# Optimization experiments

Hardware: AMD Instinct MI355X
Metric: run time of the kernel (lower is better)

Reference implementation:

```python
import jax, jax.numpy as jnp
import numpy as np

STRIDE = 1
PAD = 1
K = 3  # kernel size


def setup_inputs() -> dict:
    key = jax.random.key(0)
    k1, k2, k3, k4 = jax.random.split(key, 4)
    B, C, H, W, O = 4, 256, 64, 64, 256
    x = jax.random.normal(k1, (B, C, H, W), jnp.float32)
    offset = jax.random.normal(k2, (B, 2 * K * K, H, W), jnp.float32)
    mask = jax.random.uniform(k3, (B, K * K, H, W), jnp.float32)
    # kaiming-ish scale for the conv weight
    weight = jax.random.normal(k4, (O, C, K, K), jnp.float32) / np.float32(np.sqrt(C * K * K))
    return {"x": x, "offset": offset, "mask": mask, "weight": weight}


def _deform_conv2d(x, offset, mask, weight, stride=STRIDE, pad=PAD):
    """Modulated deformable conv v2 (torchvision deform_conv2d semantics)."""
    B, C, H, W = x.shape
    O, _, Kh, Kw = weight.shape
    KK = Kh * Kw
    Ho = (H + 2 * pad - Kh) // stride + 1
    Wo = (W + 2 * pad - Kw) // stride + 1

    # offset layout: [B, 2*KK, Ho, Wo], pairs are (dy, dx) per kernel tap
    off = offset.reshape(B, KK, 2, Ho, Wo)
    dy, dx = off[:, :, 0], off[:, :, 1]  # [B, KK, Ho, Wo]

    ki = (jnp.arange(KK) // Kw).astype(x.dtype)  # kernel row per tap
    kj = (jnp.arange(KK) % Kw).astype(x.dtype)   # kernel col per tap
    base_y = (jnp.arange(Ho) * stride - pad).astype(x.dtype)
    base_x = (jnp.arange(Wo) * stride - pad).astype(x.dtype)

    # sampling positions [B, KK, Ho, Wo]
    py = base_y[None, None, :, None] + ki[None, :, None, None] + dy
    px = base_x[None, None, None, :] + kj[None, :, None, None] + dx

    y0 = jnp.floor(py)
    x0 = jnp.floor(px)
    wy = py - y0  # fractional weights
    wx = px - x0
    y0i = y0.astype(jnp.int32)
    x0i = x0.astype(jnp.int32)

    x_bhwc = jnp.transpose(x, (0, 2, 3, 1))  # [B, H, W, C] for gathers
    b_idx = jnp.arange(B)[:, None, None, None]

    def gather(yi, xi):
        # zero outside the image (zero-padding bilinear sampling)
        valid = (yi >= 0) & (yi < H) & (xi >= 0) & (xi < W)
        v = x_bhwc[b_idx, jnp.clip(yi, 0, H - 1), jnp.clip(xi, 0, W - 1)]  # [B,KK,Ho,Wo,C]
        return v * valid[..., None].astype(x.dtype)

    one = jnp.asarray(1, x.dtype)
    sampled = (gather(y0i, x0i) * ((one - wy) * (one - wx))[..., None]
               + gather(y0i, x0i + 1) * ((one - wy) * wx)[..., None]
               + gather(y0i + 1, x0i) * (wy * (one - wx))[..., None]
               + gather(y0i + 1, x0i + 1) * (wy * wx)[..., None])

    sampled = sampled * mask.reshape(B, KK, Ho, Wo)[..., None]  # modulation

    # weighted accumulation == implicit GEMM over (c, kk)
    return jnp.einsum('bkhwc,ock->bohw', sampled, weight.reshape(O, C, KK))


def reference(x, offset, mask, weight):
    return _deform_conv2d(x, offset, mask, weight)
```

## Files before the change

### kernel.cpp

```cpp
#include <hip/hip_runtime.h>
#include <hip/hip_bf16.h>

#define CN 256
#define HN 64
#define WN 64
#define ON 256
#define KKN 9
#define HWN 4096
#define KDIM 2304
#define KC 288

using frag_ab = __attribute__((ext_vector_type(8))) short;
using frag_cd = __attribute__((ext_vector_type(4))) float;
using short4v = __attribute__((ext_vector_type(4))) short;
using int4v   = __attribute__((ext_vector_type(4))) int;
using float4v = __attribute__((ext_vector_type(4))) float;
using float2v = __attribute__((ext_vector_type(2))) float;
using uint2v  = __attribute__((ext_vector_type(2))) unsigned;

static __device__ inline short f2bf(float f) {
    union { float f; unsigned u; } v; v.f = f;
    unsigned r = v.u + 0x7fffu + ((v.u >> 16) & 1u);
    return (short)(r >> 16);
}

__global__ __launch_bounds__(256) void prep_kernel(const float* __restrict__ x,
                                                   const float* __restrict__ wsrc,
                                                   short* __restrict__ xb16,
                                                   short* __restrict__ wtb) {
    int bidx = blockIdx.x;
    int tid  = threadIdx.x;
    if (bidx < 1024) {
        __shared__ float tile[64][65];
        int b   = bidx >> 8;
        int rem = bidx & 255;
        int c0  = (rem >> 6) * 64;
        int p0  = (rem & 63) * 64;
        int tp = tid & 63, tc = tid >> 6;
        for (int i = 0; i < 16; ++i) {
            int c = tc + i * 4;
            tile[c][tp] = x[(b * CN + c0 + c) * HWN + p0 + tp];
        }
        __syncthreads();
        int tcc = tid & 63, tpp = tid >> 6;
        for (int i = 0; i < 16; ++i) {
            int p = tpp + i * 4;
            xb16[(b * HWN + p0 + p) * CN + c0 + tcc] = f2bf(tile[tcc][p]);
        }
    } else {
        int chunk = (bidx - 1024) * 256 + tid;
        int ob  = chunk / (KC * 64);
        int rem = chunk - ob * (KC * 64);
        int kc  = rem >> 6;
        int row = rem & 63;
        int o   = ob * 64 + row;
        int kk  = kc >> 5;
        int oct = kc & 31;
        frag_ab v;
        #pragma unroll
        for (int e = 0; e < 8; ++e)
            v[e] = f2bf(wsrc[(o * CN + oct * 8 + e) * 9 + kk]);
        *(frag_ab*)&wtb[(size_t)chunk * 8] = v;
    }
}

__global__ __launch_bounds__(512, 4) void fused_kernel(const short* __restrict__ xb16,
                                                       const short* __restrict__ wtb,
                                                       const float* __restrict__ offs,
                                                       const float* __restrict__ maskp,
                                                       float* __restrict__ out) {
    __shared__ struct {
        union {
            short Ab[2][8448];
            float outb[32 * 257];
        } mix;
        int desc[2304];
    } sm;
    int tid  = threadIdx.x;
    int m0   = blockIdx.x * 32;
    int b    = m0 >> 12;
    int h    = (m0 >> 6) & 63;
    int w0   = m0 & 63;
    int wv   = __builtin_amdgcn_readfirstlane(tid >> 6);
    int lane = tid & 63;
    int q    = lane >> 4, r = lane & 15;
    int wbase = 33 * (lane >> 1) * 8 + (lane & 1) * 4;
    int lane4 = lane * 4;
    int wv4   = wv * 4;

    if (tid < 288) {
        int kk = tid >> 5;
        int m  = tid & 31;
        int wc = w0 + m;
        int p  = h * 64 + wc;
        int ki = kk / 3, kj = kk - ki * 3;
        float dy = offs[(b * 18 + 2 * kk) * HWN + p];
        float dx = offs[(b * 18 + 2 * kk + 1) * HWN + p];
        float mv = maskp[(b * 9 + kk) * HWN + p];
        float py = (float)(h - 1 + ki) + dy;
        float px = (float)(wc - 1 + kj) + dx;
        float y0f = floorf(py), x0f = floorf(px);
        float wy = py - y0f, wx = px - x0f;
        int y0 = (int)y0f, x0 = (int)x0f;
        int4v cb; float4v cw;
        #pragma unroll
        for (int cy = 0; cy < 2; ++cy)
            #pragma unroll
            for (int cx = 0; cx < 2; ++cx) {
                int yy = y0 + cy, xx = x0 + cx;
                bool valid = (yy >= 0 && yy < HN && xx >= 0 && xx < WN);
                int yc = min(max(yy, 0), HN - 1);
                int xc = min(max(xx, 0), WN - 1);
                cb[cy * 2 + cx] = ((b * HN + yc) * WN + xc) * CN;
                float wgt = (cy ? wy : 1.f - wy) * (cx ? wx : 1.f - wx) * mv;
                cw[cy * 2 + cx] = valid ? wgt : 0.f;
            }
        int* dd = &sm.desc[tid * 8];
        *(int4v*)dd       = cb;
        *(float4v*)(dd + 4) = cw;
    }
    __syncthreads();

    frag_cd acc[2][2];
    #pragma unroll
    for (int i = 0; i < 2; ++i)
        #pragma unroll
        for (int j = 0; j < 2; ++j)
            acc[i][j] = (frag_cd){0.f, 0.f, 0.f, 0.f};

    short4v stg[4][4];
    float4v cwc[4];

    auto prefetch = [&](int kk1) {
        #pragma unroll
        for (int i = 0; i < 4; ++i) {
            int dbase = (kk1 * 32 + wv4 + i) * 8;
            int4v cb = *(const int4v*)&sm.desc[dbase];
            cwc[i]   = *(const float4v*)&sm.desc[dbase + 4];
            #pragma unroll
            for (int c = 0; c < 4; ++c)
                stg[i][c] = *(const short4v*)&xb16[cb[c] + lane4];
        }
    };

    prefetch(0);

    int jb = (wv & 1) * 2;
    int ob = wv >> 1;
    for (int kk = 0; kk < KKN; ++kk) {
        short* dst = sm.mix.Ab[kk & 1];
        #pragma unroll
        for (int i = 0; i < 4; ++i) {
            float4v cw = cwc[i];
            short4v res;
            #pragma unroll
            for (int g = 0; g < 2; ++g) {
                float2v a = (float2v){0.f, 0.f};
                #pragma unroll
                for (int c = 0; c < 4; ++c) {
                    uint2v uv = __builtin_bit_cast(uint2v, stg[i][c]);
                    unsigned uu = uv[g];
                    float2v f;
                    f.x = __builtin_bit_cast(float, uu << 16);
                    f.y = __builtin_bit_cast(float, uu & 0xffff0000u);
                    a += f * cw[c];
                }
                __hip_bfloat162 p2 = __float22bfloat162_rn(make_float2(a.x, a.y));
                res[2 * g]     = *(short*)&p2.x;
                res[2 * g + 1] = *(short*)&p2.y;
            }
            *(short4v*)&dst[wbase + (wv4 + i) * 8] = res;
        }
        if (kk < 8) prefetch(kk + 1);
        __syncthreads();
        #pragma unroll
        for (int ks = 0; ks < 8; ++ks) {
            frag_ab af[2], bf[2];
            #pragma unroll
            for (int i = 0; i < 2; ++i)
                af[i] = *(const frag_ab*)
                    &dst[(33 * (ks * 4 + q) + i * 16 + r) * 8];
            #pragma unroll
            for (int j = 0; j < 2; ++j)
                bf[j] = *(const frag_ab*)
                    &wtb[(((size_t)ob * KC + kk * 32 + ks * 4 + q) * 64
                          + (jb + j) * 16 + r) * 8];
            __builtin_amdgcn_s_setprio(1);
            #pragma unroll
            for (int i = 0; i < 2; ++i)
                #pragma unroll
                for (int j = 0; j < 2; ++j)
                    acc[i][j] = __builtin_amdgcn_mfma_f32_16x16x32_bf16(
                        af[i], bf[j], acc[i][j], 0, 0, 0);
            __builtin_amdgcn_s_setprio(0);
        }
    }
    __syncthreads();

    #pragma unroll
    for (int i = 0; i < 2; ++i)
        #pragma unroll
        for (int j = 0; j < 2; ++j) {
            int ml = i * 16 + q * 4;
            int ol = wv * 32 + j * 16 + r;
            sm.mix.outb[(ml + 0) * 257 + ol] = acc[i][j][0];
            sm.mix.outb[(ml + 1) * 257 + ol] = acc[i][j][1];
            sm.mix.outb[(ml + 2) * 257 + ol] = acc[i][j][2];
            sm.mix.outb[(ml + 3) * 257 + ol] = acc[i][j][3];
        }
    __syncthreads();
    {
        int ww = tid & 31;
        int og = tid >> 5;
        #pragma unroll
        for (int oo = 0; oo < 16; ++oo) {
            int o = oo * 16 + og;
            out[(((size_t)b * ON + o) * HN + h) * WN + w0 + ww] =
                sm.mix.outb[ww * 257 + o];
        }
    }
}

extern "C" void kernel_launch(void* const* d_in, const int* in_sizes, int n_in,
                              void* d_out, int out_size, void* d_ws, size_t ws_size,
                              hipStream_t stream) {
    const float* x      = (const float*)d_in[0];
    const float* offset = (const float*)d_in[1];
    const float* mask   = (const float*)d_in[2];
    const float* weight = (const float*)d_in[3];
    float* out = (float*)d_out;

    short* xb16 = (short*)d_ws;
    short* wtb  = (short*)((char*)d_ws + 8388608);

    hipLaunchKernelGGL(prep_kernel,  dim3(1312), dim3(256), 0, stream,
                       x, weight, xb16, wtb);
    hipLaunchKernelGGL(fused_kernel, dim3(512),  dim3(512), 0, stream,
                       xb16, wtb, offset, mask, out);
}
```

Before: 121.3 us.

## Enlarge fused block to a full 64-pixel row with 16 waves and register-prefetched weights

Each block of the fused kernel now covers a whole 64-pixel output row with 1024 threads (16 waves), and the grid drops from 512 to 256 blocks. Each wave now owns 16 output channels across all 64 pixels, so one weight fragment feeds four MFMAs instead of two. Weight fragments are double-buffered in registers, loaded two k-steps ahead, and the pre-MFMA __syncthreads becomes an LDS-only waitcnt plus a raw barrier. The cost is double the LDS per block, fewer blocks for the 256 CUs, and heavier register pressure under the 1024-thread launch bound.

```diff
diff --git a/kernel.cpp b/kernel.cpp
--- a/kernel.cpp
+++ b/kernel.cpp
@@ -64,41 +64,39 @@
     }
 }
 
-__global__ __launch_bounds__(512, 4) void fused_kernel(const short* __restrict__ xb16,
-                                                       const short* __restrict__ wtb,
-                                                       const float* __restrict__ offs,
-                                                       const float* __restrict__ maskp,
-                                                       float* __restrict__ out) {
+__global__ __launch_bounds__(1024, 4) void fused_kernel(const short* __restrict__ xb16,
+                                                        const short* __restrict__ wtb,
+                                                        const float* __restrict__ offs,
+                                                        const float* __restrict__ maskp,
+                                                        float* __restrict__ out) {
     __shared__ struct {
         union {
-            short Ab[2][8448];
-            float outb[32 * 257];
+            short Ab[2][16640];
+            float outb[64 * 257];
         } mix;
-        int desc[2304];
+        int desc[4608];
     } sm;
     int tid  = threadIdx.x;
-    int m0   = blockIdx.x * 32;
+    int m0   = blockIdx.x * 64;
     int b    = m0 >> 12;
     int h    = (m0 >> 6) & 63;
-    int w0   = m0 & 63;
     int wv   = __builtin_amdgcn_readfirstlane(tid >> 6);
     int lane = tid & 63;
     int q    = lane >> 4, r = lane & 15;
-    int wbase = 33 * (lane >> 1) * 8 + (lane & 1) * 4;
+    int wbase = 65 * (lane >> 1) * 8 + (lane & 1) * 4;
     int lane4 = lane * 4;
     int wv4   = wv * 4;
 
-    if (tid < 288) {
-        int kk = tid >> 5;
-        int m  = tid & 31;
-        int wc = w0 + m;
-        int p  = h * 64 + wc;
+    if (tid < 576) {
+        int kk = tid >> 6;
+        int m  = tid & 63;
+        int p  = h * 64 + m;
         int ki = kk / 3, kj = kk - ki * 3;
         float dy = offs[(b * 18 + 2 * kk) * HWN + p];
         float dx = offs[(b * 18 + 2 * kk + 1) * HWN + p];
         float mv = maskp[(b * 9 + kk) * HWN + p];
         float py = (float)(h - 1 + ki) + dy;
-        float px = (float)(wc - 1 + kj) + dx;
+        float px = (float)(m - 1 + kj) + dx;
         float y0f = floorf(py), x0f = floorf(px);
         float wy = py - y0f, wx = px - x0f;
         int y0 = (int)y0f, x0 = (int)x0f;
@@ -121,12 +119,10 @@
     }
     __syncthreads();
 
-    frag_cd acc[2][2];
+    frag_cd acc[4];
     #pragma unroll
-    for (int i = 0; i < 2; ++i)
-        #pragma unroll
-        for (int j = 0; j < 2; ++j)
-            acc[i][j] = (frag_cd){0.f, 0.f, 0.f, 0.f};
+    for (int i = 0; i < 4; ++i)
+        acc[i] = (frag_cd){0.f, 0.f, 0.f, 0.f};
 
     short4v stg[4][4];
     float4v cwc[4];
@@ -134,7 +130,7 @@
     auto prefetch = [&](int kk1) {
         #pragma unroll
         for (int i = 0; i < 4; ++i) {
-            int dbase = (kk1 * 32 + wv4 + i) * 8;
+            int dbase = (kk1 * 64 + wv4 + i) * 8;
             int4v cb = *(const int4v*)&sm.desc[dbase];
             cwc[i]   = *(const float4v*)&sm.desc[dbase + 4];
             #pragma unroll
@@ -143,12 +139,21 @@
         }
     };
 
+    int ob   = wv >> 2;
+    int orow = (wv & 3) * 16;
+    auto ld_bf = [&](int kk, int ks) {
+        return *(const frag_ab*)
+            &wtb[(((size_t)ob * KC + kk * 32 + ks * 4 + q) * 64
+                  + orow + r) * 8];
+    };
+
     prefetch(0);
 
-    int jb = (wv & 1) * 2;
-    int ob = wv >> 1;
     for (int kk = 0; kk < KKN; ++kk) {
         short* dst = sm.mix.Ab[kk & 1];
+        frag_ab bfx[2];
+        bfx[0] = ld_bf(kk, 0);
+        bfx[1] = ld_bf(kk, 1);
         #pragma unroll
         for (int i = 0; i < 4; ++i) {
             float4v cw = cwc[i];
@@ -172,50 +177,46 @@
             *(short4v*)&dst[wbase + (wv4 + i) * 8] = res;
         }
         if (kk < 8) prefetch(kk + 1);
-        __syncthreads();
+        asm volatile("s_waitcnt lgkmcnt(0)" ::: "memory");
+        __builtin_amdgcn_s_barrier();
+        asm volatile("" ::: "memory");
         #pragma unroll
         for (int ks = 0; ks < 8; ++ks) {
-            frag_ab af[2], bf[2];
-            #pragma unroll
-            for (int i = 0; i < 2; ++i)
+            const int cur = ks & 1;
+            frag_ab af[4];
+            #pragma unroll
+            for (int i = 0; i < 4; ++i)
                 af[i] = *(const frag_ab*)
-                    &dst[(33 * (ks * 4 + q) + i * 16 + r) * 8];
-            #pragma unroll
-            for (int j = 0; j < 2; ++j)
-                bf[j] = *(const frag_ab*)
-                    &wtb[(((size_t)ob * KC + kk * 32 + ks * 4 + q) * 64
-                          + (jb + j) * 16 + r) * 8];
+                    &dst[(65 * (ks * 4 + q) + i * 16 + r) * 8];
             __builtin_amdgcn_s_setprio(1);
             #pragma unroll
-            for (int i = 0; i < 2; ++i)
-                #pragma unroll
-                for (int j = 0; j < 2; ++j)
-                    acc[i][j] = __builtin_amdgcn_mfma_f32_16x16x32_bf16(
-                        af[i], bf[j], acc[i][j], 0, 0, 0);
+            for (int i = 0; i < 4; ++i)
+                acc[i] = __builtin_amdgcn_mfma_f32_16x16x32_bf16(
+                    af[i], bfx[cur], acc[i], 0, 0, 0);
             __builtin_amdgcn_s_setprio(0);
+            if (ks < 6)
+                bfx[cur] = ld_bf(kk, ks + 2);
         }
     }
     __syncthreads();
 
     #pragma unroll
-    for (int i = 0; i < 2; ++i)
-        #pragma unroll
-        for (int j = 0; j < 2; ++j) {
-            int ml = i * 16 + q * 4;
-            int ol = wv * 32 + j * 16 + r;
-            sm.mix.outb[(ml + 0) * 257 + ol] = acc[i][j][0];
-            sm.mix.outb[(ml + 1) * 257 + ol] = acc[i][j][1];
-            sm.mix.outb[(ml + 2) * 257 + ol] = acc[i][j][2];
-            sm.mix.outb[(ml + 3) * 257 + ol] = acc[i][j][3];
-        }
+    for (int i = 0; i < 4; ++i) {
+        int ml = i * 16 + q * 4;
+        int ol = wv * 16 + r;
+        sm.mix.outb[(ml + 0) * 257 + ol] = acc[i][0];
+        sm.mix.outb[(ml + 1) * 257 + ol] = acc[i][1];
+        sm.mix.outb[(ml + 2) * 257 + ol] = acc[i][2];
+        sm.mix.outb[(ml + 3) * 257 + ol] = acc[i][3];
+    }
     __syncthreads();
     {
-        int ww = tid & 31;
-        int og = tid >> 5;
+        int ww = tid & 63;
+        int og = tid >> 6;
         #pragma unroll
         for (int oo = 0; oo < 16; ++oo) {
             int o = oo * 16 + og;
-            out[(((size_t)b * ON + o) * HN + h) * WN + w0 + ww] =
+            out[(((size_t)b * ON + o) * HN + h) * WN + ww] =
                 sm.mix.outb[ww * 257 + o];
         }
     }
@@ -233,8 +234,8 @@
     short* xb16 = (short*)d_ws;
     short* wtb  = (short*)((char*)d_ws + 8388608);
 
-    hipLaunchKernelGGL(prep_kernel,  dim3(1312), dim3(256), 0, stream,
+    hipLaunchKernelGGL(prep_kernel,  dim3(1312), dim3(256),  0, stream,
                        x, weight, xb16, wtb);
-    hipLaunchKernelGGL(fused_kernel, dim3(512),  dim3(512), 0, stream,
+    hipLaunchKernelGGL(fused_kernel, dim3(256),  dim3(1024), 0, stream,
                        xb16, wtb, offset, mask, out);
 }
```

New measurement: 117.7 us. -2.9%, faster.
